# Kernel optimization log

Hardware: AMD Instinct MI355X
Metric: run time of the kernel (lower is better)

Reference implementation:

```python
import jax, jax.numpy as jnp
import numpy as np

# tcnn Hash-grid config from TropicalHashGrid.__init__ defaults
L = 16          # n_levels
F = 2           # n_features_per_level
T = 19          # log2_hashmap_size
N_MIN = 16      # base_resolution
N_MAX = 2048
SCALE = 1.0
HASHMAP = 1 << T
B = 2.0 ** (np.log2(N_MAX * SCALE / N_MIN) / (L - 1))  # per-level scale
PRIMES = np.array([1, 2654435761, 805459861], dtype=np.uint32)
# 8 trilinear corner offsets in {0,1}^3
CORNERS = np.stack(np.meshgrid(*([np.arange(2)] * 3), indexing='ij'), axis=-1).reshape(8, 3)
N_POINTS = 2 ** 21


def _level_encode(x, tbl, scale, res, dense):
    """One hash-grid level: x [N,3], tbl [HASHMAP,F] -> [N,F]."""
    pos = x * scale + 0.5                      # tcnn convention
    pf = jnp.floor(pos)
    frac = pos - pf                            # [N,3]
    grid = pf.astype(jnp.int32)                # [N,3]
    idx = grid[:, None, :] + jnp.asarray(CORNERS, jnp.int32)[None]  # [N,8,3]
    if dense:
        # coarse level fits densely: stride indexing x + y*res + z*res^2
        idx = jnp.minimum(idx, res - 1)
        flat = idx[..., 0] + idx[..., 1] * res + idx[..., 2] * (res * res)
    else:
        # spatial hash: xor of coordinate * prime, masked to table size
        u = idx.astype(jnp.uint32)
        flat = ((u[..., 0] * PRIMES[0]) ^ (u[..., 1] * PRIMES[1]) ^ (u[..., 2] * PRIMES[2]))
        flat = (flat & jnp.uint32(HASHMAP - 1)).astype(jnp.int32)
    feats = tbl[flat]                          # [N,8,F] gather
    c = jnp.asarray(CORNERS, jnp.float32)
    w = jnp.prod(jnp.where(c[None] > 0, frac[:, None, :], 1.0 - frac[:, None, :]), axis=-1)  # [N,8]
    return jnp.einsum('nc,ncf->nf', w, feats)  # trilinear blend


def setup_inputs() -> dict:
    key = jax.random.key(0)
    k1, k2 = jax.random.split(key)
    x = jax.random.uniform(k1, (N_POINTS, 3), dtype=jnp.float32)  # coords in [0,1)^3
    # hash table params (tcnn inits ~U(-1e-4,1e-4); scaled randn equivalent scale)
    table = jax.random.normal(k2, (L, HASHMAP, F), dtype=jnp.float32) * 1e-4
    return {"x": x, "table": table}


def reference(x, table):
    outs = []
    for l in range(L):
        scale = float(N_MIN * (B ** l) - 1.0)   # grid_scale per tcnn/_marks
        res = int(np.ceil(scale)) + 1
        dense = (res ** 3) <= HASHMAP
        outs.append(_level_encode(x, table[l], scale, res, dense))
    return jnp.concatenate(outs, axis=-1)        # [N, L*F]
```

## Files before the change

### kernel.cpp

```cpp
#include <hip/hip_runtime.h>
#include <cstdint>
#include <cmath>


typedef float f32x2 __attribute__((ext_vector_type(2)));
typedef float f32x4 __attribute__((ext_vector_type(4)));

#define NLEVELS 16
#define HASHMAP (1 << 19)
#define HMASK ((uint32_t)(HASHMAP - 1))
#define PRIME_Y 2654435761u
#define PRIME_Z 805459861u

struct HGParams {
    float scale[NLEVELS];
    int   res[NLEVELS];
    int   dense[NLEVELS];
    int   dpk_off[NLEVELS];
    int   bypass[NLEVELS];
};

__device__ __forceinline__ f32x4 gload4_sc0(const f32x4* p) {
    f32x4 v;
    asm volatile("global_load_dwordx4 %0, %1, off sc0" : "=&v"(v) : "v"(p));
    return v;
}
__device__ __forceinline__ f32x2 gload2_sc0(const f32x2* p) {
    f32x2 v;
    asm volatile("global_load_dwordx2 %0, %1, off sc0" : "=&v"(v) : "v"(p));
    return v;
}

__global__ __launch_bounds__(256) void repack_dense_k(
    const f32x2* __restrict__ table, f32x4* __restrict__ dpk, HGParams p)
{
    const int l = blockIdx.y;
    if (!p.dense[l] || p.dpk_off[l] < 0) return;
    const int res = p.res[l];
    const int res3 = res * res * res;
    const f32x2* __restrict__ src = table + (size_t)l * HASHMAP;
    f32x4* __restrict__ dst = dpk + p.dpk_off[l];
    for (int k = blockIdx.x * 256 + threadIdx.x; k < res3; k += gridDim.x * 256) {
        const f32x2 a = src[k];
        const f32x2 b = src[k + 1];
        f32x4 v; v.x = a.x; v.y = a.y; v.z = b.x; v.w = b.y;
        dst[k] = v;
    }
}

__global__ __launch_bounds__(256) void hashgrid_level(
    const float* __restrict__ x,
    const float* __restrict__ table,
    const f32x4* __restrict__ dpk,
    f32x2* __restrict__ dst,
    HGParams p,
    int npoints,
    size_t stride_l,
    size_t stride_n)
{
    __shared__ float sx[768];
    const int tid = threadIdx.x;
    const int base = blockIdx.x << 8;
    const int l = blockIdx.y;

    const int total = npoints * 3;
#pragma unroll
    for (int k = 0; k < 3; ++k) {
        const int li = tid + (k << 8);
        const int gi = base * 3 + li;
        sx[li] = (gi < total) ? x[gi] : 0.0f;
    }
    __syncthreads();

    const int n = base + tid;
    if (n >= npoints) return;

    const float scale = p.scale[l];
    const int   res   = p.res[l];
    const bool  dense = (p.dense[l] != 0);

    const float px = sx[tid * 3 + 0] * scale + 0.5f;
    const float py = sx[tid * 3 + 1] * scale + 0.5f;
    const float pz = sx[tid * 3 + 2] * scale + 0.5f;
    const float fx = floorf(px), fy = floorf(py), fz = floorf(pz);
    const float rx = px - fx,  ry = py - fy,  rz = pz - fz;
    const int ix = (int)fx, iy = (int)fy, iz = (int)fz;

    const f32x2* __restrict__ tbl =
        (const f32x2*)table + (size_t)l * (size_t)HASHMAP;

    const float wx0 = 1.0f - rx, wx1 = rx;
    const float wy_[2] = {1.0f - ry, ry};
    const float wz_[2] = {1.0f - rz, rz};

    float ax = 0.0f, ay = 0.0f;

    if (dense) {
        const int rm = res - 1;
        const int x0 = min(ix, rm), x1 = min(ix + 1, rm);
        const int y0 = min(iy, rm), y1 = min(iy + 1, rm);
        const int z0 = min(iz, rm), z1 = min(iz + 1, rm);
        const int r2 = res * res;
        const int ys[2] = {y0 * res, y1 * res};
        const int zs[2] = {z0 * r2,  z1 * r2};
        const int d = x1 - x0;
        if (dpk && p.dpk_off[l] >= 0) {
            const f32x4* __restrict__ dt = dpk + p.dpk_off[l];
            f32x4 f4[4];
            if (p.bypass[l]) {
#pragma unroll
                for (int c = 0; c < 4; ++c)
                    f4[c] = gload4_sc0(dt + x0 + ys[(c >> 1) & 1] + zs[c & 1]);
                asm volatile("s_waitcnt vmcnt(0)"
                             : "+v"(f4[0]), "+v"(f4[1]), "+v"(f4[2]), "+v"(f4[3]));
            } else {
#pragma unroll
                for (int c = 0; c < 4; ++c)
                    f4[c] = dt[x0 + ys[(c >> 1) & 1] + zs[c & 1]];
            }
#pragma unroll
            for (int c = 0; c < 4; ++c) {
                const f32x2 c0 = f4[c].xy;
                const f32x2 c1 = d ? f4[c].zw : f4[c].xy;
                const float wyz = wy_[(c >> 1) & 1] * wz_[c & 1];
                ax += wyz * (wx0 * c0.x + wx1 * c1.x);
                ay += wyz * (wx0 * c0.y + wx1 * c1.y);
            }
        } else {
            f32x2 f0[4], f1[4];
#pragma unroll
            for (int c = 0; c < 4; ++c) {
                const int b = ys[(c >> 1) & 1] + zs[c & 1];
                f0[c] = tbl[x0 + b];
                f1[c] = tbl[x1 + b];
            }
#pragma unroll
            for (int c = 0; c < 4; ++c) {
                const float wyz = wy_[(c >> 1) & 1] * wz_[c & 1];
                ax += wyz * (wx0 * f0[c].x + wx1 * f1[c].x);
                ay += wyz * (wx0 * f0[c].y + wx1 * f1[c].y);
            }
        }
    } else {
        const uint32_t ux = (uint32_t)ix;
        const uint32_t hy[2] = {(uint32_t)iy * PRIME_Y, (uint32_t)(iy + 1) * PRIME_Y};
        const uint32_t hz[2] = {(uint32_t)iz * PRIME_Z, (uint32_t)(iz + 1) * PRIME_Z};
        const f32x4* __restrict__ t4 = (const f32x4*)tbl;

        uint32_t H0[4], H1[4];
#pragma unroll
        for (int c = 0; c < 4; ++c) {
            const uint32_t hyz = hy[(c >> 1) & 1] ^ hz[c & 1];
            H0[c] = (ux ^ hyz) & HMASK;
            H1[c] = ((ux + 1u) ^ hyz) & HMASK;
        }
        f32x4 f4[4];
#pragma unroll
        for (int c = 0; c < 4; ++c) f4[c] = gload4_sc0(t4 + (H0[c] >> 1));

        f32x2 o[4];
#pragma unroll
        for (int c = 0; c < 4; ++c) { o[c].x = 0.0f; o[c].y = 0.0f; }
        const bool odd = (ux & 1u) != 0u;
        if (odd) {
#pragma unroll
            for (int c = 0; c < 4; ++c) o[c] = gload2_sc0(tbl + H1[c]);
        }
        asm volatile("s_waitcnt vmcnt(0)"
                     : "+v"(f4[0]), "+v"(f4[1]), "+v"(f4[2]), "+v"(f4[3]),
                       "+v"(o[0]), "+v"(o[1]), "+v"(o[2]), "+v"(o[3]));

#pragma unroll
        for (int c = 0; c < 4; ++c) {
            const f32x2 c0 = (H0[c] & 1u) ? f4[c].zw : f4[c].xy;
            const f32x2 cw = (H0[c] & 1u) ? f4[c].xy : f4[c].zw;
            const f32x2 c1 = odd ? o[c] : cw;
            const float wyz = wy_[(c >> 1) & 1] * wz_[c & 1];
            ax += wyz * (wx0 * c0.x + wx1 * c1.x);
            ay += wyz * (wx0 * c0.y + wx1 * c1.y);
        }
    }

    f32x2 acc; acc.x = ax; acc.y = ay;
    __builtin_nontemporal_store(acc, dst + (size_t)l * stride_l + (size_t)n * stride_n);
}

__global__ __launch_bounds__(256) void transpose_out(
    const f32x4* __restrict__ ws4,
    f32x4* __restrict__ out4,
    int npoints)
{
    __shared__ f32x2 tile[NLEVELS][130];
    const int tid = threadIdx.x;
    const int base = blockIdx.x << 7;
    const int np2 = npoints >> 1;

#pragma unroll
    for (int k = 0; k < 4; ++k) {
        const int flat = tid + (k << 8);
        const int l  = flat >> 6;
        const int pr = flat & 63;
        const int gp = (base >> 1) + pr;
        if (gp < np2) {
            const f32x4 v = __builtin_nontemporal_load(ws4 + (size_t)l * np2 + gp);
            tile[l][2 * pr]     = v.xy;
            tile[l][2 * pr + 1] = v.zw;
        }
    }
    __syncthreads();

#pragma unroll
    for (int k = 0; k < 4; ++k) {
        const int flat = tid + (k << 8);
        const int nl = flat >> 3;
        const int c  = flat & 7;
        const int nn = base + nl;
        if (nn < npoints) {
            const f32x2 a = tile[2 * c][nl];
            const f32x2 b = tile[2 * c + 1][nl];
            f32x4 v; v.x = a.x; v.y = a.y; v.z = b.x; v.w = b.y;
            __builtin_nontemporal_store(v, out4 + (size_t)nn * 8 + c);
        }
    }
}

extern "C" void kernel_launch(void* const* d_in, const int* in_sizes, int n_in,
                              void* d_out, int out_size, void* d_ws, size_t ws_size,
                              hipStream_t stream) {
    const float* x     = (const float*)d_in[0];
    const float* table = (const float*)d_in[1];
    float* out         = (float*)d_out;
    const int npoints  = in_sizes[0] / 3;

    HGParams p;
    const double B = pow(2.0, 7.0 / 15.0);
    int dpk_total = 0;
    int max_res3 = 0;
    for (int l = 0; l < NLEVELS; ++l) {
        const double s = 16.0 * pow(B, (double)l) - 1.0;
        p.scale[l] = (float)s;
        const int res = (int)ceil(s) + 1;
        p.res[l] = res;
        const long long r3 = (long long)res * res * res;
        p.dense[l] = (r3 <= (long long)HASHMAP) ? 1 : 0;
        if (p.dense[l]) {
            p.dpk_off[l] = dpk_total;
            dpk_total += (int)r3;
            if ((int)r3 > max_res3) max_res3 = (int)r3;
            p.bypass[l] = (r3 * 16 > (256 << 10)) ? 1 : 0;
        } else {
            p.dpk_off[l] = -1;
            p.bypass[l] = 1;
        }
    }

    const size_t need_main = (size_t)npoints * NLEVELS * sizeof(f32x2);
    const size_t need_dpk  = (size_t)dpk_total * sizeof(f32x4);

    const bool ws_main = (ws_size >= need_main) && ((npoints & 1) == 0);
    size_t dpk_byte_off = ws_main ? need_main : 0;
    const bool use_dpk = (ws_size >= dpk_byte_off + need_dpk) && dpk_total > 0;

    f32x4* dpk = use_dpk ? (f32x4*)((char*)d_ws + dpk_byte_off) : nullptr;
    if (use_dpk) {
        const dim3 gr((max_res3 + 255) / 256, NLEVELS);
        repack_dense_k<<<gr, 256, 0, stream>>>((const f32x2*)table, dpk, p);
    }

    const dim3 g1((npoints + 255) / 256, NLEVELS);
    if (ws_main) {
        hashgrid_level<<<g1, 256, 0, stream>>>(
            x, table, dpk, (f32x2*)d_ws, p, npoints, (size_t)npoints, (size_t)1);
        const int nb2 = (npoints + 127) / 128;
        transpose_out<<<nb2, 256, 0, stream>>>(
            (const f32x4*)d_ws, (f32x4*)out, npoints);
    } else {
        hashgrid_level<<<g1, 256, 0, stream>>>(
            x, table, dpk, (f32x2*)out, p, npoints, (size_t)1, (size_t)NLEVELS);
    }
}
```

Measured before the change: 1.133 ms.

## Repack hash tables to scaled fp16 and pack 2x2 dense corners per entry

Each call now converts the hashed-level tables to fp16, scaled by 1024 to stay clear of the subnormal range, packed four entries per 16-byte word. The dense levels are repacked so one 16-byte entry holds the four x/y-neighbour corners in fp16. The main kernel then needs two loads per point on dense levels, and usually four loads on hashed levels because x and x+1 land in the same 16-byte word unless x mod 4 is 3. This halves table footprint to improve cache hit rates and cut gather traffic. In exchange it adds two repack kernels per call and loses some accuracy from fp16 rounding, and it drops the sc0 cache-bypass loads.

```diff
diff --git a/kernel.cpp b/kernel.cpp
--- a/kernel.cpp
+++ b/kernel.cpp
@@ -3,32 +3,89 @@
 #include <cmath>
 
 
-typedef float f32x2 __attribute__((ext_vector_type(2)));
-typedef float f32x4 __attribute__((ext_vector_type(4)));
+typedef float    f32x2 __attribute__((ext_vector_type(2)));
+typedef float    f32x4 __attribute__((ext_vector_type(4)));
+typedef uint32_t u32x2 __attribute__((ext_vector_type(2)));
+typedef uint32_t u32x4 __attribute__((ext_vector_type(4)));
+typedef _Float16 h16x2 __attribute__((ext_vector_type(2)));
 
 #define NLEVELS 16
 #define HASHMAP (1 << 19)
 #define HMASK ((uint32_t)(HASHMAP - 1))
 #define PRIME_Y 2654435761u
 #define PRIME_Z 805459861u
+#define F16SCALE 1024.0f
+#define F16UNSCALE (1.0f / 1024.0f)
 
 struct HGParams {
     float scale[NLEVELS];
     int   res[NLEVELS];
     int   dense[NLEVELS];
     int   dpk_off[NLEVELS];
-    int   bypass[NLEVELS];
+    int   hq_off[NLEVELS];
+    int   dq_off[NLEVELS];
 };
 
-__device__ __forceinline__ f32x4 gload4_sc0(const f32x4* p) {
-    f32x4 v;
-    asm volatile("global_load_dwordx4 %0, %1, off sc0" : "=&v"(v) : "v"(p));
-    return v;
-}
-__device__ __forceinline__ f32x2 gload2_sc0(const f32x2* p) {
-    f32x2 v;
-    asm volatile("global_load_dwordx2 %0, %1, off sc0" : "=&v"(v) : "v"(p));
-    return v;
+__device__ __forceinline__ uint32_t sel4(u32x4 q, uint32_t k) {
+    const uint32_t a = (k & 1u) ? q.y : q.x;
+    const uint32_t b = (k & 1u) ? q.w : q.z;
+    return (k & 2u) ? b : a;
+}
+__device__ __forceinline__ void unpack_h2(uint32_t w, float& lo, float& hi) {
+    const h16x2 h = __builtin_bit_cast(h16x2, w);
+    lo = (float)h.x; hi = (float)h.y;
+}
+__device__ __forceinline__ uint32_t pack_h2(float a, float b) {
+    h16x2 h; h.x = (_Float16)a; h.y = (_Float16)b;
+    return __builtin_bit_cast(uint32_t, h);
+}
+
+__global__ __launch_bounds__(256) void repack_hashed_f16(
+    const f32x4* __restrict__ table2, uint32_t* __restrict__ hqw, HGParams p)
+{
+    const int l = blockIdx.y;
+    if (p.hq_off[l] < 0) return;
+    const f32x4* __restrict__ src = table2 + (size_t)l * (HASHMAP / 2);
+    u32x2* __restrict__ dst = (u32x2*)(hqw + (size_t)p.hq_off[l] * 4);
+    for (int k = blockIdx.x * 256 + threadIdx.x; k < HASHMAP / 2;
+         k += gridDim.x * 256) {
+        const f32x4 v = src[k];
+        u32x2 w;
+        w.x = pack_h2(v.x * F16SCALE, v.y * F16SCALE);
+        w.y = pack_h2(v.z * F16SCALE, v.w * F16SCALE);
+        dst[k] = w;
+    }
+}
+
+__global__ __launch_bounds__(256) void repack_dense_f16(
+    const f32x2* __restrict__ table, u32x4* __restrict__ dqt, HGParams p)
+{
+    const int l = blockIdx.y;
+    if (p.dq_off[l] < 0) return;
+    const int res = p.res[l];
+    const int rm = res - 1;
+    const int r2 = res * res;
+    const int res3 = r2 * res;
+    const f32x2* __restrict__ src = table + (size_t)l * HASHMAP;
+    u32x4* __restrict__ dst = dqt + p.dq_off[l];
+    for (int k = blockIdx.x * 256 + threadIdx.x; k < res3;
+         k += gridDim.x * 256) {
+        const int x = k % res;
+        const int t = k / res;
+        const int y = t % res;
+        const int dx = (x < rm) ? 1 : 0;
+        const int dy = (y < rm) ? res : 0;
+        const f32x2 e00 = src[k];
+        const f32x2 e10 = src[k + dx];
+        const f32x2 e01 = src[k + dy];
+        const f32x2 e11 = src[k + dx + dy];
+        u32x4 w;
+        w.x = pack_h2(e00.x * F16SCALE, e00.y * F16SCALE);
+        w.y = pack_h2(e10.x * F16SCALE, e10.y * F16SCALE);
+        w.z = pack_h2(e01.x * F16SCALE, e01.y * F16SCALE);
+        w.w = pack_h2(e11.x * F16SCALE, e11.y * F16SCALE);
+        dst[k] = w;
+    }
 }
 
 __global__ __launch_bounds__(256) void repack_dense_k(
@@ -52,6 +109,8 @@
     const float* __restrict__ x,
     const float* __restrict__ table,
     const f32x4* __restrict__ dpk,
+    const u32x4* __restrict__ hq,
+    const u32x4* __restrict__ dq,
     f32x2* __restrict__ dst,
     HGParams p,
     int npoints,
@@ -94,58 +153,81 @@
     const float wz_[2] = {1.0f - rz, rz};
 
     float ax = 0.0f, ay = 0.0f;
+    float osc = 1.0f;
 
     if (dense) {
         const int rm = res - 1;
-        const int x0 = min(ix, rm), x1 = min(ix + 1, rm);
-        const int y0 = min(iy, rm), y1 = min(iy + 1, rm);
+        const int x0 = min(ix, rm);
+        const int y0 = min(iy, rm);
         const int z0 = min(iz, rm), z1 = min(iz + 1, rm);
         const int r2 = res * res;
-        const int ys[2] = {y0 * res, y1 * res};
-        const int zs[2] = {z0 * r2,  z1 * r2};
-        const int d = x1 - x0;
-        if (dpk && p.dpk_off[l] >= 0) {
-            const f32x4* __restrict__ dt = dpk + p.dpk_off[l];
-            f32x4 f4[4];
-            if (p.bypass[l]) {
-#pragma unroll
-                for (int c = 0; c < 4; ++c)
-                    f4[c] = gload4_sc0(dt + x0 + ys[(c >> 1) & 1] + zs[c & 1]);
-                asm volatile("s_waitcnt vmcnt(0)"
-                             : "+v"(f4[0]), "+v"(f4[1]), "+v"(f4[2]), "+v"(f4[3]));
-            } else {
+        if (dq && p.dq_off[l] >= 0) {
+            osc = F16UNSCALE;
+            const u32x4* __restrict__ dt = dq + p.dq_off[l];
+            const int b = x0 + y0 * res;
+            const u32x4 qa = dt[b + z0 * r2];
+            const u32x4 qb = dt[b + z1 * r2];
+            const float wy0 = wy_[0], wy1 = wy_[1];
+            float a00x, a00y, a10x, a10y, a01x, a01y, a11x, a11y;
+            unpack_h2(qa.x, a00x, a00y);
+            unpack_h2(qa.y, a10x, a10y);
+            unpack_h2(qa.z, a01x, a01y);
+            unpack_h2(qa.w, a11x, a11y);
+            const float bax = wy0 * (wx0 * a00x + wx1 * a10x)
+                            + wy1 * (wx0 * a01x + wx1 * a11x);
+            const float bay = wy0 * (wx0 * a00y + wx1 * a10y)
+                            + wy1 * (wx0 * a01y + wx1 * a11y);
+            float b00x, b00y, b10x, b10y, b01x, b01y, b11x, b11y;
+            unpack_h2(qb.x, b00x, b00y);
+            unpack_h2(qb.y, b10x, b10y);
+            unpack_h2(qb.z, b01x, b01y);
+            unpack_h2(qb.w, b11x, b11y);
+            const float bbx = wy0 * (wx0 * b00x + wx1 * b10x)
+                            + wy1 * (wx0 * b01x + wx1 * b11x);
+            const float bby = wy0 * (wx0 * b00y + wx1 * b10y)
+                            + wy1 * (wx0 * b01y + wx1 * b11y);
+            ax = wz_[0] * bax + wz_[1] * bbx;
+            ay = wz_[0] * bay + wz_[1] * bby;
+        } else {
+            const int x1 = min(ix + 1, rm);
+            const int yy1 = min(iy + 1, rm);
+            const int ys[2] = {y0 * res, yy1 * res};
+            const int zs[2] = {z0 * r2,  z1 * r2};
+            const int d = x1 - x0;
+            if (dpk && p.dpk_off[l] >= 0) {
+                const f32x4* __restrict__ dt = dpk + p.dpk_off[l];
+                f32x4 f4[4];
 #pragma unroll
                 for (int c = 0; c < 4; ++c)
                     f4[c] = dt[x0 + ys[(c >> 1) & 1] + zs[c & 1]];
-            }
-#pragma unroll
-            for (int c = 0; c < 4; ++c) {
-                const f32x2 c0 = f4[c].xy;
-                const f32x2 c1 = d ? f4[c].zw : f4[c].xy;
-                const float wyz = wy_[(c >> 1) & 1] * wz_[c & 1];
-                ax += wyz * (wx0 * c0.x + wx1 * c1.x);
-                ay += wyz * (wx0 * c0.y + wx1 * c1.y);
-            }
-        } else {
-            f32x2 f0[4], f1[4];
-#pragma unroll
-            for (int c = 0; c < 4; ++c) {
-                const int b = ys[(c >> 1) & 1] + zs[c & 1];
-                f0[c] = tbl[x0 + b];
-                f1[c] = tbl[x1 + b];
-            }
-#pragma unroll
-            for (int c = 0; c < 4; ++c) {
-                const float wyz = wy_[(c >> 1) & 1] * wz_[c & 1];
-                ax += wyz * (wx0 * f0[c].x + wx1 * f1[c].x);
-                ay += wyz * (wx0 * f0[c].y + wx1 * f1[c].y);
+#pragma unroll
+                for (int c = 0; c < 4; ++c) {
+                    const f32x2 c0 = f4[c].xy;
+                    const f32x2 c1 = d ? f4[c].zw : f4[c].xy;
+                    const float wyz = wy_[(c >> 1) & 1] * wz_[c & 1];
+                    ax += wyz * (wx0 * c0.x + wx1 * c1.x);
+                    ay += wyz * (wx0 * c0.y + wx1 * c1.y);
+                }
+            } else {
+                f32x2 f0[4], f1[4];
+#pragma unroll
+                for (int c = 0; c < 4; ++c) {
+                    const int b = ys[(c >> 1) & 1] + zs[c & 1];
+                    f0[c] = tbl[x0 + b];
+                    f1[c] = tbl[x1 + b];
+                }
+#pragma unroll
+                for (int c = 0; c < 4; ++c) {
+                    const float wyz = wy_[(c >> 1) & 1] * wz_[c & 1];
+                    ax += wyz * (wx0 * f0[c].x + wx1 * f1[c].x);
+                    ay += wyz * (wx0 * f0[c].y + wx1 * f1[c].y);
+                }
             }
         }
     } else {
         const uint32_t ux = (uint32_t)ix;
         const uint32_t hy[2] = {(uint32_t)iy * PRIME_Y, (uint32_t)(iy + 1) * PRIME_Y};
         const uint32_t hz[2] = {(uint32_t)iz * PRIME_Z, (uint32_t)(iz + 1) * PRIME_Z};
-        const f32x4* __restrict__ t4 = (const f32x4*)tbl;
 
         uint32_t H0[4], H1[4];
 #pragma unroll
@@ -154,34 +236,57 @@
             H0[c] = (ux ^ hyz) & HMASK;
             H1[c] = ((ux + 1u) ^ hyz) & HMASK;
         }
-        f32x4 f4[4];
-#pragma unroll
-        for (int c = 0; c < 4; ++c) f4[c] = gload4_sc0(t4 + (H0[c] >> 1));
-
-        f32x2 o[4];
-#pragma unroll
-        for (int c = 0; c < 4; ++c) { o[c].x = 0.0f; o[c].y = 0.0f; }
-        const bool odd = (ux & 1u) != 0u;
-        if (odd) {
-#pragma unroll
-            for (int c = 0; c < 4; ++c) o[c] = gload2_sc0(tbl + H1[c]);
-        }
-        asm volatile("s_waitcnt vmcnt(0)"
-                     : "+v"(f4[0]), "+v"(f4[1]), "+v"(f4[2]), "+v"(f4[3]),
-                       "+v"(o[0]), "+v"(o[1]), "+v"(o[2]), "+v"(o[3]));
-
-#pragma unroll
-        for (int c = 0; c < 4; ++c) {
-            const f32x2 c0 = (H0[c] & 1u) ? f4[c].zw : f4[c].xy;
-            const f32x2 cw = (H0[c] & 1u) ? f4[c].xy : f4[c].zw;
-            const f32x2 c1 = odd ? o[c] : cw;
-            const float wyz = wy_[(c >> 1) & 1] * wz_[c & 1];
-            ax += wyz * (wx0 * c0.x + wx1 * c1.x);
-            ay += wyz * (wx0 * c0.y + wx1 * c1.y);
-        }
-    }
-
-    f32x2 acc; acc.x = ax; acc.y = ay;
+
+        if (hq && p.hq_off[l] >= 0) {
+            osc = F16UNSCALE;
+            const u32x4* __restrict__ ht = hq + p.hq_off[l];
+            u32x4 q0[4];
+#pragma unroll
+            for (int c = 0; c < 4; ++c) q0[c] = ht[H0[c] >> 2];
+            const bool straddle = ((ux & 3u) == 3u);
+            u32x4 q1[4];
+            if (straddle) {
+#pragma unroll
+                for (int c = 0; c < 4; ++c) q1[c] = ht[H1[c] >> 2];
+            }
+#pragma unroll
+            for (int c = 0; c < 4; ++c) {
+                const uint32_t e0 = sel4(q0[c], H0[c] & 3u);
+                uint32_t e1;
+                if (straddle) e1 = sel4(q1[c], H1[c] & 3u);
+                else          e1 = sel4(q0[c], H1[c] & 3u);
+                float c0x, c0y, c1x, c1y;
+                unpack_h2(e0, c0x, c0y);
+                unpack_h2(e1, c1x, c1y);
+                const float wyz = wy_[(c >> 1) & 1] * wz_[c & 1];
+                ax += wyz * (wx0 * c0x + wx1 * c1x);
+                ay += wyz * (wx0 * c0y + wx1 * c1y);
+            }
+        } else {
+            const f32x4* __restrict__ t4 = (const f32x4*)tbl;
+            f32x4 f4[4];
+#pragma unroll
+            for (int c = 0; c < 4; ++c) f4[c] = t4[H0[c] >> 1];
+            f32x2 c1v[4];
+            if (ux & 1u) {
+#pragma unroll
+                for (int c = 0; c < 4; ++c) c1v[c] = tbl[H1[c]];
+            } else {
+#pragma unroll
+                for (int c = 0; c < 4; ++c)
+                    c1v[c] = (H0[c] & 1u) ? f4[c].xy : f4[c].zw;
+            }
+#pragma unroll
+            for (int c = 0; c < 4; ++c) {
+                const f32x2 c0 = (H0[c] & 1u) ? f4[c].zw : f4[c].xy;
+                const float wyz = wy_[(c >> 1) & 1] * wz_[c & 1];
+                ax += wyz * (wx0 * c0.x + wx1 * c1v[c].x);
+                ay += wyz * (wx0 * c0.y + wx1 * c1v[c].y);
+            }
+        }
+    }
+
+    f32x2 acc; acc.x = ax * osc; acc.y = ay * osc;
     __builtin_nontemporal_store(acc, dst + (size_t)l * stride_l + (size_t)n * stride_n);
 }
 
@@ -235,6 +340,8 @@
     HGParams p;
     const double B = pow(2.0, 7.0 / 15.0);
     int dpk_total = 0;
+    int dq_total = 0;
+    int hq_total = 0;
     int max_res3 = 0;
     for (int l = 0; l < NLEVELS; ++l) {
         const double s = 16.0 * pow(B, (double)l) - 1.0;
@@ -244,38 +351,69 @@
         const long long r3 = (long long)res * res * res;
         p.dense[l] = (r3 <= (long long)HASHMAP) ? 1 : 0;
         if (p.dense[l]) {
-            p.dpk_off[l] = dpk_total;
-            dpk_total += (int)r3;
+            p.dpk_off[l] = dpk_total;  dpk_total += (int)r3;
+            p.dq_off[l]  = dq_total;   dq_total  += (int)r3;
+            p.hq_off[l]  = -1;
             if ((int)r3 > max_res3) max_res3 = (int)r3;
-            p.bypass[l] = (r3 * 16 > (256 << 10)) ? 1 : 0;
         } else {
             p.dpk_off[l] = -1;
-            p.bypass[l] = 1;
+            p.dq_off[l]  = -1;
+            p.hq_off[l]  = hq_total;   hq_total  += HASHMAP / 4;
         }
     }
 
     const size_t need_main = (size_t)npoints * NLEVELS * sizeof(f32x2);
-    const size_t need_dpk  = (size_t)dpk_total * sizeof(f32x4);
-
     const bool ws_main = (ws_size >= need_main) && ((npoints & 1) == 0);
-    size_t dpk_byte_off = ws_main ? need_main : 0;
-    const bool use_dpk = (ws_size >= dpk_byte_off + need_dpk) && dpk_total > 0;
-
-    f32x4* dpk = use_dpk ? (f32x4*)((char*)d_ws + dpk_byte_off) : nullptr;
-    if (use_dpk) {
-        const dim3 gr((max_res3 + 255) / 256, NLEVELS);
-        repack_dense_k<<<gr, 256, 0, stream>>>((const f32x2*)table, dpk, p);
+    const size_t off0 = ws_main ? need_main : 0;
+
+    const size_t hq_bytes = (size_t)hq_total * 16;
+    const size_t dq_bytes = (size_t)dq_total * 16;
+    const bool tierA = (ws_size >= off0 + hq_bytes + dq_bytes);
+
+    const u32x4* hq = nullptr;
+    const u32x4* dq = nullptr;
+    const f32x4* dpk = nullptr;
+
+    if (tierA) {
+        uint32_t* hqw = (uint32_t*)((char*)d_ws + off0);
+        u32x4*    dqt = (u32x4*)((char*)d_ws + off0 + hq_bytes);
+        hq = (const u32x4*)hqw;
+        dq = dqt;
+        {
+            const dim3 gr(1024, NLEVELS);
+            repack_hashed_f16<<<gr, 256, 0, stream>>>(
+                (const f32x4*)table, hqw, p);
+        }
+        {
+            const dim3 gr((max_res3 + 255) / 256, NLEVELS);
+            repack_dense_f16<<<gr, 256, 0, stream>>>(
+                (const f32x2*)table, dqt, p);
+        }
+    } else {
+        for (int l = 0; l < NLEVELS; ++l) { p.hq_off[l] = -1; p.dq_off[l] = -1; }
+        const size_t need_dpk = (size_t)dpk_total * sizeof(f32x4);
+        const bool use_dpk = (ws_size >= off0 + need_dpk) && dpk_total > 0;
+        if (use_dpk) {
+            f32x4* dpkw = (f32x4*)((char*)d_ws + off0);
+            dpk = dpkw;
+            const dim3 gr((max_res3 + 255) / 256, NLEVELS);
+            repack_dense_k<<<gr, 256, 0, stream>>>((const f32x2*)table, dpkw, p);
+        } else {
+            for (int l = 0; l < NLEVELS; ++l) p.dpk_off[l] = -1;
+        }
     }
 
     const dim3 g1((npoints + 255) / 256, NLEVELS);
     if (ws_main) {
         hashgrid_level<<<g1, 256, 0, stream>>>(
-            x, table, dpk, (f32x2*)d_ws, p, npoints, (size_t)npoints, (size_t)1);
+            x, table, dpk, hq, dq, (f32x2*)d_ws, p, npoints,
+            (size_t)npoints, (size_t)1);
         const int nb2 = (npoints + 127) / 128;
         transpose_out<<<nb2, 256, 0, stream>>>(
             (const f32x4*)d_ws, (f32x4*)out, npoints);
     } else {
         hashgrid_level<<<g1, 256, 0, stream>>>(
-            x, table, dpk, (f32x2*)out, p, npoints, (size_t)1, (size_t)NLEVELS);
-    }
-}
+            x, table, dpk, hq, dq, (f32x2*)out, p, npoints,
+            (size_t)1, (size_t)NLEVELS);
+    }
+}
```

Result: faster. 929.3 us (-18.0%).
